# Optimization experiments

Measured on AMD Instinct MI355X. Metric: run time of the kernel, lower is better.

The kernel has to match this reference:

```python
import jax, jax.numpy as jnp
import numpy as np

B, S, D, H, M = 2, 2048, 1024, 16, 40
DH = D // H  # 64
L = S + M    # kv length after memory concat


def setup_inputs() -> dict:
    key = jax.random.key(0)
    ks = jax.random.split(key, 20)
    s = 1.0 / np.sqrt(D)
    inp = {
        'v': jax.random.normal(ks[0], (B, S, D), jnp.float32),
        'k': jax.random.normal(ks[1], (B, S, D), jnp.float32),
        'q': jax.random.normal(ks[2], (B, S, D), jnp.float32),
        # additive binary mask (1 = masked out), broadcast over heads
        'mask': jax.random.randint(ks[3], (B, 1, S, L), 0, 2).astype(jnp.float32),
        'Wq': jax.random.normal(ks[4], (D, D), jnp.float32) * s,
        'bq': jnp.zeros((D,), jnp.float32),
        'Wk': jax.random.normal(ks[5], (D, D), jnp.float32) * s,
        'bk': jnp.zeros((D,), jnp.float32),
        'Wv': jax.random.normal(ks[6], (D, D), jnp.float32) * s,
        'bv': jnp.zeros((D,), jnp.float32),
        'k_memory': jax.random.normal(ks[7], (1, M, D), jnp.float32) * (1.0 / np.sqrt(DH)),
        'v_memory': jax.random.normal(ks[8], (1, M, D), jnp.float32) * (1.0 / np.sqrt(M)),
        'Wkm': jax.random.normal(ks[9], (D, D), jnp.float32) * s,
        'bkm': jnp.zeros((D,), jnp.float32),
        'Wvm': jax.random.normal(ks[10], (D, D), jnp.float32) * s,
        'bvm': jnp.zeros((D,), jnp.float32),
        'Wo': jax.random.normal(ks[11], (D, D), jnp.float32) * s,
        'bo': jnp.zeros((D,), jnp.float32),
    }
    return inp


def _split_heads(x):
    # [B, T, D] -> [B, H, T, DH]
    b, t, _ = x.shape
    return x.reshape(b, t, H, DH).transpose(0, 2, 1, 3)


def reference(v, k, q, mask, Wq, bq, Wk, bk, Wv, bv, k_memory, v_memory,
              Wkm, bkm, Wvm, bvm, Wo, bo):
    qp = q @ Wq + bq
    kp = k @ Wk + bk
    vp = v @ Wv + bv
    km = (k_memory @ Wkm + bkm)  # [1, M, D]
    vm = (v_memory @ Wvm + bvm)  # [1, M, D]
    kc = jnp.concatenate([kp, jnp.broadcast_to(km, (kp.shape[0], M, D))], axis=1)
    vc = jnp.concatenate([vp, jnp.broadcast_to(vm, (vp.shape[0], M, D))], axis=1)
    qh, kh, vh = _split_heads(qp), _split_heads(kc), _split_heads(vc)
    # scores: [B, H, S, L]
    scores = jnp.einsum('bhqd,bhkd->bhqk', qh, kh) / np.sqrt(DH)
    scores = scores + mask * (-1e9)
    attn = jax.nn.softmax(scores, axis=-1)
    ctx = jnp.einsum('bhqk,bhkd->bhqd', attn, vh)  # [B, H, S, DH]
    ctx = ctx.transpose(0, 2, 1, 3).reshape(ctx.shape[0], S, D)
    out = ctx @ Wo + bo
    return (out, attn)
```

## Files before the change

### kernel.cpp

```cpp
#include <hip/hip_runtime.h>
#include <hip/hip_bf16.h>

typedef __attribute__((ext_vector_type(8))) short short8v;
typedef __attribute__((ext_vector_type(4))) short short4v;
typedef __attribute__((ext_vector_type(4))) float f32x4;

constexpr int B_ = 2, S_ = 2048, H_ = 16, MM_ = 40;
constexpr int L_ = S_ + MM_;
constexpr int LP_ = 2112;
constexpr int NT_ = 33;
constexpr float QSCALE = 0.18033688011112042f;

struct S2 { short hi, lo; };
__device__ __forceinline__ S2 split2(float f) {
    unsigned u = __builtin_bit_cast(unsigned, f);
    short hi = (short)(u >> 16);
    float fh = __builtin_bit_cast(float, u & 0xFFFF0000u);
    float fl = f - fh;
    short lo = (short)(__builtin_bit_cast(unsigned, fl) >> 16);
    return {hi, lo};
}
__device__ __forceinline__ short f2bh(float f) {
    unsigned u = __builtin_bit_cast(unsigned, f);
    u = (u + 0x7FFFu + ((u >> 16) & 1u)) >> 16;
    return (short)u;
}
__device__ __forceinline__ f32x4 mfma16(short8v a, short8v b, f32x4 c) {
    return __builtin_amdgcn_mfma_f32_16x16x32_bf16(a, b, c, 0, 0, 0);
}
__device__ __forceinline__ unsigned cvt_pk_bf16(float a, float b) {
    unsigned r;
    asm("v_cvt_pk_bf16_f32 %0, %1, %2" : "=v"(r) : "v"(a), "v"(b));
    return r;
}

__global__ __launch_bounds__(256) void wsplit6_kernel(
    const float* __restrict__ W0, const float* __restrict__ W1,
    const float* __restrict__ W2, const float* __restrict__ W3,
    const float* __restrict__ W4, const float* __restrict__ W5,
    short* __restrict__ WT)
{
    const float* Ws[6] = {W0, W1, W2, W3, W4, W5};
    const float* W = Ws[blockIdx.z];
    short* WTh = WT + (size_t)blockIdx.z * 2097152;
    short* WTl = WTh + 1048576;
    __shared__ float T[64][68];
    const int t = threadIdx.x;
    const int k0 = blockIdx.x * 64, n0 = blockIdx.y * 64;
    {
        int r = t >> 2, c = (t & 3) * 16;
        const float* src = W + (size_t)(k0 + r) * 1024 + n0 + c;
        *(float4*)&T[r][c + 0]  = *(const float4*)(src + 0);
        *(float4*)&T[r][c + 4]  = *(const float4*)(src + 4);
        *(float4*)&T[r][c + 8]  = *(const float4*)(src + 8);
        *(float4*)&T[r][c + 12] = *(const float4*)(src + 12);
    }
    __syncthreads();
    {
        int n = t >> 2, ks = (t & 3) * 16;
        short8v h0, h1, l0, l1;
#pragma unroll
        for (int j = 0; j < 8; ++j) {
            S2 a = split2(T[ks + j][n]);     h0[j] = a.hi; l0[j] = a.lo;
            S2 b = split2(T[ks + 8 + j][n]); h1[j] = b.hi; l1[j] = b.lo;
        }
        size_t dst = (size_t)(n0 + n) * 1024 + k0 + ks;
        *(short8v*)(WTh + dst) = h0;  *(short8v*)(WTh + dst + 8) = h1;
        *(short8v*)(WTl + dst) = l0;  *(short8v*)(WTl + dst + 8) = l1;
    }
}

template<int ASRC>
__device__ __forceinline__ void gemm_core(
    const float* __restrict__ Af, const short* __restrict__ Ahg,
    const short* __restrict__ Alg, const short* __restrict__ WTh,
    const short* __restrict__ WTl, const float* __restrict__ bias,
    float bscale, float scale,
    short* __restrict__ Oh, short* __restrict__ Ol, float* __restrict__ Of,
    int M, int RPB, int TD, int loff, int omode, int bx, int by,
    int kbeg, int kend)
{
    __shared__ short Ah[128][40];
    __shared__ short Al[128][40];
    __shared__ short Bh[128][40];
    __shared__ short Bl[128][40];
    const int tid = threadIdx.x;
    const int lane = tid & 63, wid = tid >> 6;
    const int wr = wid >> 1, wc = wid & 1;
    const int row0 = by * 128, col0 = bx * 128;
    const int sr = tid >> 1, sc = (tid & 1) << 4;

    f32x4 acc[4][4] = {};

    for (int k0 = kbeg; k0 < kend; k0 += 32) {
        if (ASRC == 0) {
            float f[16];
            int gr = row0 + sr;
            if (gr < M) {
                const float* ap = Af + (size_t)gr * 1024 + k0 + sc;
                float4 a0 = *(const float4*)(ap + 0);
                float4 a1 = *(const float4*)(ap + 4);
                float4 a2 = *(const float4*)(ap + 8);
                float4 a3 = *(const float4*)(ap + 12);
                f[0]=a0.x; f[1]=a0.y; f[2]=a0.z; f[3]=a0.w;
                f[4]=a1.x; f[5]=a1.y; f[6]=a1.z; f[7]=a1.w;
                f[8]=a2.x; f[9]=a2.y; f[10]=a2.z; f[11]=a2.w;
                f[12]=a3.x; f[13]=a3.y; f[14]=a3.z; f[15]=a3.w;
            } else {
#pragma unroll
                for (int j = 0; j < 16; ++j) f[j] = 0.f;
            }
            short8v h0, h1, l0, l1;
#pragma unroll
            for (int j = 0; j < 8; ++j) {
                S2 s = split2(f[j]); h0[j] = s.hi; l0[j] = s.lo;
            }
#pragma unroll
            for (int j = 0; j < 8; ++j) {
                S2 s = split2(f[8 + j]); h1[j] = s.hi; l1[j] = s.lo;
            }
            *(short8v*)&Ah[sr][sc] = h0; *(short8v*)&Ah[sr][sc + 8] = h1;
            *(short8v*)&Al[sr][sc] = l0; *(short8v*)&Al[sr][sc + 8] = l1;
        } else {
            const short* ah = Ahg + (size_t)(row0 + sr) * 1024 + k0 + sc;
            const short* al = Alg + (size_t)(row0 + sr) * 1024 + k0 + sc;
            *(short8v*)&Ah[sr][sc]     = *(const short8v*)ah;
            *(short8v*)&Ah[sr][sc + 8] = *(const short8v*)(ah + 8);
            *(short8v*)&Al[sr][sc]     = *(const short8v*)al;
            *(short8v*)&Al[sr][sc + 8] = *(const short8v*)(al + 8);
        }
        {
            const short* bh = WTh + (size_t)(col0 + sr) * 1024 + k0 + sc;
            const short* bl = WTl + (size_t)(col0 + sr) * 1024 + k0 + sc;
            *(short8v*)&Bh[sr][sc]     = *(const short8v*)bh;
            *(short8v*)&Bh[sr][sc + 8] = *(const short8v*)(bh + 8);
            *(short8v*)&Bl[sr][sc]     = *(const short8v*)bl;
            *(short8v*)&Bl[sr][sc + 8] = *(const short8v*)(bl + 8);
        }
        __syncthreads();
        const int kof = (lane >> 4) << 3;
        const int ar = lane & 15;
        short8v afh[4], afl[4], bfh[4], bfl[4];
#pragma unroll
        for (int i = 0; i < 4; ++i) {
            afh[i] = *(const short8v*)&Ah[wr * 64 + i * 16 + ar][kof];
            afl[i] = *(const short8v*)&Al[wr * 64 + i * 16 + ar][kof];
            bfh[i] = *(const short8v*)&Bh[wc * 64 + i * 16 + ar][kof];
            bfl[i] = *(const short8v*)&Bl[wc * 64 + i * 16 + ar][kof];
        }
#pragma unroll
        for (int i = 0; i < 4; ++i)
#pragma unroll
            for (int j = 0; j < 4; ++j) {
                acc[i][j] = mfma16(afh[i], bfh[j], acc[i][j]);
                acc[i][j] = mfma16(afh[i], bfl[j], acc[i][j]);
                acc[i][j] = mfma16(afl[i], bfh[j], acc[i][j]);
            }
        __syncthreads();
    }

#pragma unroll
    for (int i = 0; i < 4; ++i) {
#pragma unroll
        for (int j = 0; j < 4; ++j) {
            int colb = col0 + wc * 64 + j * 16 + (lane & 15);
            float bv = bias[colb] * bscale;
            int rowb = row0 + wr * 64 + i * 16 + ((lane >> 4) << 2);
            if (omode == 2) {
                if (rowb < M) {
                    int bb = rowb / RPB, tt = rowb % RPB;
                    int hh = colb >> 6, dh = colb & 63;
                    short4v hs;
#pragma unroll
                    for (int r = 0; r < 4; ++r)
                        hs[r] = f2bh((acc[i][j][r] + bv) * scale);
                    size_t dst = ((size_t)(bb * H_ + hh) * 64 + dh) * LP_ + loff + tt;
                    *(short4v*)(Oh + dst) = hs;
                }
            } else {
#pragma unroll
                for (int r = 0; r < 4; ++r) {
                    int row = rowb + r;
                    if (row < M) {
                        float o = (acc[i][j][r] + bv) * scale;
                        int bb = row / RPB, tt = row % RPB;
                        if (omode == 0) {
                            Of[((size_t)bb * TD + loff + tt) * 1024 + colb] = o;
                        } else {
                            int hh = colb >> 6, dh = colb & 63;
                            size_t dst = ((size_t)(bb * H_ + hh) * TD + loff + tt) * 64 + dh;
                            S2 s = split2(o);
                            Oh[dst] = s.hi; Ol[dst] = s.lo;
                        }
                    }
                }
            }
        }
    }
}

__global__ __launch_bounds__(256) void qkv_gemm(
    const float* __restrict__ q_in, const float* __restrict__ k_in,
    const float* __restrict__ v_in, const float* __restrict__ kmem,
    const float* __restrict__ vmem, const short* __restrict__ WT,
    const float* __restrict__ bq, const float* __restrict__ bk,
    const float* __restrict__ bv, const float* __restrict__ bkm,
    const float* __restrict__ bvm,
    short* __restrict__ Qh, short* __restrict__ Ql,
    short* __restrict__ Kh, short* __restrict__ Kl, short* __restrict__ Vh,
    const float* __restrict__ mask, unsigned* __restrict__ mp)
{
    const int z = blockIdx.z;
    if (z == 0) {
        const int blk = blockIdx.y * 8 + blockIdx.x;
        for (int rr = 0; rr < 16; ++rr) {
            const int row = blk * 16 + rr;
            const float* mr = mask + (size_t)row * L_;
            unsigned* orow = mp + (size_t)row * 68;
            for (int wd = threadIdx.x; wd < 66; wd += 256) {
                int l0 = wd * 32;
                unsigned bits = 0u;
                int lim = (wd < 65) ? 32 : 8;
                for (int j = 0; j < lim; j += 4) {
                    float4 m4 = *(const float4*)(mr + l0 + j);
                    bits |= ((unsigned)(m4.x != 0.f)) << (j + 0);
                    bits |= ((unsigned)(m4.y != 0.f)) << (j + 1);
                    bits |= ((unsigned)(m4.z != 0.f)) << (j + 2);
                    bits |= ((unsigned)(m4.w != 0.f)) << (j + 3);
                }
                if (wd == 65) bits |= 0xFFFFFF00u;
                orow[wd] = bits;
            }
        }
        for (int k = threadIdx.x; k < 192; k += 256) {
            int g = blk * 192 + k;
            int rd = g / 24, l = L_ + g % 24;
            Vh[(size_t)rd * LP_ + l] = 0;
        }
        return;
    }
    if (z >= 4) {
        if (blockIdx.y != 0) return;
        const int which = (z - 4) >> 1, b = (z - 4) & 1;
        const float* A = which ? vmem : kmem;
        const short* WTh = WT + (size_t)(3 + which) * 2097152;
        const short* WTl = WTh + 1048576;
        const float* bias = which ? bvm : bkm;
        short* Oh = which ? (Vh + (size_t)b * H_ * 64 * LP_)
                          : (Kh + (size_t)b * H_ * LP_ * 64);
        short* Ol = which ? nullptr : (Kl + (size_t)b * H_ * LP_ * 64);
        gemm_core<0>(A, nullptr, nullptr, WTh, WTl, bias, 1.0f, 1.0f,
                     Oh, Ol, nullptr, 40, 40, LP_, S_, which ? 2 : 1,
                     blockIdx.x, 0, 0, 1024);
        return;
    }
    const int g = z - 1;
    const float* A = (g == 0) ? q_in : (g == 1) ? k_in : v_in;
    const short* WTh = WT + (size_t)g * 2097152;
    const short* WTl = WTh + 1048576;
    const float* bias = (g == 0) ? bq : (g == 1) ? bk : bv;
    float scale = (g == 0) ? QSCALE : 1.0f;
    short* Oh = (g == 0) ? Qh : (g == 1) ? Kh : Vh;
    short* Ol = (g == 0) ? Ql : Kl;
    int omode = (g == 2) ? 2 : 1;
    int TD = (g == 0) ? S_ : LP_;
    gemm_core<0>(A, nullptr, nullptr, WTh, WTl, bias, 1.0f, scale,
                 Oh, Ol, nullptr, 4096, 2048, TD, 0, omode,
                 blockIdx.x, blockIdx.y, 0, 1024);
}

__global__ __launch_bounds__(256) void out_gemm(
    const short* __restrict__ Ch, const short* __restrict__ Cl,
    const short* __restrict__ WT, const float* __restrict__ bo,
    float* __restrict__ Po0, float* __restrict__ Po1)
{
    const int z = blockIdx.z;
    const short* WTh = WT + (size_t)5 * 2097152;
    gemm_core<1>(nullptr, Ch, Cl, WTh, WTh + 1048576, bo,
                 z == 0 ? 1.0f : 0.0f, 1.0f,
                 nullptr, nullptr, z == 0 ? Po0 : Po1, 4096, 2048, S_, 0, 0,
                 blockIdx.x, blockIdx.y, z * 512, z * 512 + 512);
}

__global__ __launch_bounds__(256) void add_out(
    const float* __restrict__ Po0, const float* __restrict__ Po1,
    float* __restrict__ outp)
{
    int i = (blockIdx.x * 256 + threadIdx.x) * 4;
    float4 a = *(const float4*)(Po0 + i);
    float4 b = *(const float4*)(Po1 + i);
    a.x += b.x; a.y += b.y; a.z += b.z; a.w += b.w;
    *(float4*)(outp + i) = a;
}

__global__ __launch_bounds__(256) void attn4_kernel(
    const short* __restrict__ Qh, const short* __restrict__ Ql,
    const short* __restrict__ Kh, const short* __restrict__ Kl,
    const short* __restrict__ Vh, const unsigned* __restrict__ mp,
    float* __restrict__ attn,
    short* __restrict__ Ch, short* __restrict__ Cl)
{
    __shared__ short KhB[2][64][64];
    __shared__ short KlB[2][64][64];
    __shared__ short VB[64][64];
    __shared__ short Ph[4][16][68];

    const int id = blockIdx.x;
    const int wg = (id & 7) * 64 + (id >> 3);
    const int bh = wg >> 4, qb2 = wg & 15;
    const int b = bh >> 4, h = bh & 15;
    const int lane = threadIdx.x & 63, w = threadIdx.x >> 6;
    const int lq = lane & 15, hi = lane >> 4;
    const int sw = lq & 7;
    const int q0A = qb2 * 128 + w * 16;
    const int q0B = q0A + 64;

    const char* kh_g = (const char*)(Kh + (size_t)bh * LP_ * 64);
    const char* kl_g = (const char*)(Kl + (size_t)bh * LP_ * 64);
    const char* v_g  = (const char*)(Vh + (size_t)bh * 64 * LP_);

    auto stage_k = [&](int buf, int tt) {
#pragma unroll
        for (int i = 0; i < 2; ++i) {
            int o = w * 2048 + i * 1024 + lane * 16;
            int r = o >> 7, c = (o >> 4) & 7;
            int cs = c ^ (r & 7);
            const char* sh = kh_g + (size_t)tt * 8192 + r * 128 + cs * 16;
            const char* sl = kl_g + (size_t)tt * 8192 + r * 128 + cs * 16;
            __builtin_amdgcn_global_load_lds((const void*)sh,
                (void*)((char*)&KhB[buf][0][0] + w * 2048 + i * 1024), 16, 0, 0);
            __builtin_amdgcn_global_load_lds((const void*)sl,
                (void*)((char*)&KlB[buf][0][0] + w * 2048 + i * 1024), 16, 0, 0);
        }
    };
    auto stage_v = [&](int tt) {
#pragma unroll
        for (int i = 0; i < 2; ++i) {
            int o = w * 2048 + i * 1024 + lane * 16;
            int dh = o >> 7, c = (o >> 4) & 7;
            int cs = c ^ (dh & 7);
            const char* src = v_g + (size_t)dh * (LP_ * 2) + (size_t)tt * 128 + cs * 16;
            __builtin_amdgcn_global_load_lds((const void*)src,
                (void*)((char*)&VB[0][0] + w * 2048 + i * 1024), 16, 0, 0);
        }
    };

    const size_t qbA = ((size_t)bh * S_ + q0A + lq) * 64 + hi * 8;
    const size_t qbB = ((size_t)bh * S_ + q0B + lq) * 64 + hi * 8;
    const short8v qh0A = *(const short8v*)(Qh + qbA);
    const short8v qh1A = *(const short8v*)(Qh + qbA + 32);
    const short8v ql0A = *(const short8v*)(Ql + qbA);
    const short8v ql1A = *(const short8v*)(Ql + qbA + 32);
    const short8v qh0B = *(const short8v*)(Qh + qbB);
    const short8v qh1B = *(const short8v*)(Qh + qbB + 32);
    const short8v ql0B = *(const short8v*)(Ql + qbB);
    const short8v ql1B = *(const short8v*)(Ql + qbB + 32);
    const unsigned* mrowA = mp + ((size_t)b * S_ + q0A + lq) * 68;
    const unsigned* mrowB = mp + ((size_t)b * S_ + q0B + lq) * 68;

    const int dr = lane >> 2, dc = lane & 3;
    short* dbaseA = (short*)(attn + ((size_t)bh * S_ + q0A + dr) * L_);
    short* dbaseB = (short*)(attn + ((size_t)bh * S_ + q0B + dr) * L_);

    float smA = 0.f, smB = 0.f;
    f32x4 pvA[4] = {};
    f32x4 pvB[4] = {};

    stage_k(0, 0);
    stage_v(0);
    __syncthreads();

    int cur = 0;
    for (int t = 0; t < NT_; ++t) {
        if (t < NT_ - 1) stage_k(cur ^ 1, t + 1);

        const short8v* kp = (const short8v*)&KhB[cur][0][0];
        const short8v* lp = (const short8v*)&KlB[cur][0][0];
        short8v kh0s[4], kh1s[4], kl0s[4], kl1s[4];
#pragma unroll
        for (int ls = 0; ls < 4; ++ls) {
            const int r = ls * 16 + lq;
            kh0s[ls] = kp[r * 8 + (hi ^ sw)];
            kh1s[ls] = kp[r * 8 + ((hi + 4) ^ sw)];
            kl0s[ls] = lp[r * 8 + (hi ^ sw)];
            kl1s[ls] = lp[r * 8 + ((hi + 4) ^ sw)];
        }
        const unsigned w0A = mrowA[2 * t], w1A = mrowA[2 * t + 1];
#pragma unroll
        for (int ls = 0; ls < 4; ++ls) {
            __builtin_amdgcn_s_setprio(1);
            f32x4 acc = {0.f, 0.f, 0.f, 0.f};
            acc = mfma16(kh0s[ls], qh0A, acc); acc = mfma16(kh1s[ls], qh1A, acc);
            acc = mfma16(kh0s[ls], ql0A, acc); acc = mfma16(kh1s[ls], ql1A, acc);
            acc = mfma16(kl0s[ls], qh0A, acc); acc = mfma16(kl1s[ls], qh1A, acc);
            __builtin_amdgcn_s_setprio(0);
            const unsigned wb = (ls & 2) ? w1A : w0A;
            const int sh = (ls & 1) * 16 + hi * 4;
            float pr[4];
#pragma unroll
            for (int r2 = 0; r2 < 4; ++r2) {
                float e = __builtin_exp2f(acc[r2]);
                pr[r2] = ((wb >> (sh + r2)) & 1u) ? 0.f : e;
            }
            smA += (pr[0] + pr[1]) + (pr[2] + pr[3]);
            *(uint2*)&Ph[w][lq][ls * 16 + hi * 4] =
                uint2{cvt_pk_bf16(pr[0], pr[1]), cvt_pk_bf16(pr[2], pr[3])};
        }
        {
            short8v v0 = *(const short8v*)&Ph[w][dr][dc * 8];
            short8v v1 = *(const short8v*)&Ph[w][dr][32 + dc * 8];
            short* dst = dbaseA + t * 64 + dc * 8;
            if (t < NT_ - 1) { *(short8v*)dst = v0; *(short8v*)(dst + 32) = v1; }
            else { *(short8v*)dst = v0; if (dc == 0) *(short8v*)(dst + 32) = v1; }
        }
        __syncthreads();
        {
            const short8v pa0 = *(const short8v*)&Ph[w][lq][hi * 8];
            const short8v pa1 = *(const short8v*)&Ph[w][lq][32 + hi * 8];
            const short8v* vp = (const short8v*)&VB[0][0];
            __builtin_amdgcn_s_setprio(1);
#pragma unroll
            for (int j = 0; j < 4; ++j)
                pvA[j] = mfma16(pa0, vp[(j * 16 + lq) * 8 + (hi ^ sw)], pvA[j]);
#pragma unroll
            for (int j = 0; j < 4; ++j)
                pvA[j] = mfma16(pa1, vp[(j * 16 + lq) * 8 + ((hi + 4) ^ sw)], pvA[j]);
            __builtin_amdgcn_s_setprio(0);
        }
        const unsigned w0B = mrowB[2 * t], w1B = mrowB[2 * t + 1];
#pragma unroll
        for (int ls = 0; ls < 4; ++ls) {
            __builtin_amdgcn_s_setprio(1);
            f32x4 acc = {0.f, 0.f, 0.f, 0.f};
            acc = mfma16(kh0s[ls], qh0B, acc); acc = mfma16(kh1s[ls], qh1B, acc);
            acc = mfma16(kh0s[ls], ql0B, acc); acc = mfma16(kh1s[ls], ql1B, acc);
            acc = mfma16(kl0s[ls], qh0B, acc); acc = mfma16(kl1s[ls], qh1B, acc);
            __builtin_amdgcn_s_setprio(0);
            const unsigned wb = (ls & 2) ? w1B : w0B;
            const int sh = (ls & 1) * 16 + hi * 4;
            float pr[4];
#pragma unroll
            for (int r2 = 0; r2 < 4; ++r2) {
                float e = __builtin_exp2f(acc[r2]);
                pr[r2] = ((wb >> (sh + r2)) & 1u) ? 0.f : e;
            }
            smB += (pr[0] + pr[1]) + (pr[2] + pr[3]);
            *(uint2*)&Ph[w][lq][ls * 16 + hi * 4] =
                uint2{cvt_pk_bf16(pr[0], pr[1]), cvt_pk_bf16(pr[2], pr[3])};
        }
        {
            short8v v0 = *(const short8v*)&Ph[w][dr][dc * 8];
            short8v v1 = *(const short8v*)&Ph[w][dr][32 + dc * 8];
            short* dst = dbaseB + t * 64 + dc * 8;
            if (t < NT_ - 1) { *(short8v*)dst = v0; *(short8v*)(dst + 32) = v1; }
            else { *(short8v*)dst = v0; if (dc == 0) *(short8v*)(dst + 32) = v1; }
        }
        {
            const short8v pa0 = *(const short8v*)&Ph[w][lq][hi * 8];
            const short8v pa1 = *(const short8v*)&Ph[w][lq][32 + hi * 8];
            const short8v* vp = (const short8v*)&VB[0][0];
            __builtin_amdgcn_s_setprio(1);
#pragma unroll
            for (int j = 0; j < 4; ++j)
                pvB[j] = mfma16(pa0, vp[(j * 16 + lq) * 8 + (hi ^ sw)], pvB[j]);
#pragma unroll
            for (int j = 0; j < 4; ++j)
                pvB[j] = mfma16(pa1, vp[(j * 16 + lq) * 8 + ((hi + 4) ^ sw)], pvB[j]);
            __builtin_amdgcn_s_setprio(0);
        }
        __syncthreads();
        if (t < NT_ - 1) stage_v(t + 1);
        cur ^= 1;
    }

    smA += __shfl_xor(smA, 16); smA += __shfl_xor(smA, 32);
    smB += __shfl_xor(smB, 16); smB += __shfl_xor(smB, 32);

#pragma unroll
    for (int r = 0; r < 4; ++r) {
        float svA = __shfl(smA, hi * 4 + r);
        float svB = __shfl(smB, hi * 4 + r);
        float ivA = svA > 0.f ? 1.0f / svA : 0.f;
        float ivB = svB > 0.f ? 1.0f / svB : 0.f;
#pragma unroll
        for (int j = 0; j < 4; ++j) {
            size_t dA = ((size_t)b * S_ + q0A + hi * 4 + r) * 1024 + h * 64 + j * 16 + lq;
            S2 sA = split2(pvA[j][r] * ivA);
            Ch[dA] = sA.hi; Cl[dA] = sA.lo;
            size_t dB = ((size_t)b * S_ + q0B + hi * 4 + r) * 1024 + h * 64 + j * 16 + lq;
            S2 sB = split2(pvB[j][r] * ivB);
            Ch[dB] = sB.hi; Cl[dB] = sB.lo;
        }
    }

    asm volatile("s_waitcnt vmcnt(0)");
#pragma unroll 1
    for (int s = 0; s < 2; ++s) {
        const int q0 = s ? q0B : q0A;
        const float smv = s ? smB : smA;
#pragma unroll 1
        for (int i = 0; i < 16; ++i) {
            float sv = __shfl(smv, i);
            float iv = sv > 0.f ? 1.0f / sv : 0.f;
            float* rowf = attn + ((size_t)bh * S_ + q0 + i) * L_;
            unsigned* rw = (unsigned*)rowf;
            unsigned u[17];
#pragma unroll
            for (int it = 0; it < 16; ++it) u[it] = rw[lane + it * 64];
            if (lane < 20) u[16] = rw[lane + 1024];
#pragma unroll
            for (int it = 0; it < 16; ++it) {
                unsigned uu = u[it];
                float2 v;
                v.x = __builtin_bit_cast(float, uu << 16) * iv;
                v.y = __builtin_bit_cast(float, uu & 0xFFFF0000u) * iv;
                *(float2*)(rowf + 2 * (lane + it * 64)) = v;
            }
            if (lane < 20) {
                unsigned uu = u[16];
                float2 v;
                v.x = __builtin_bit_cast(float, uu << 16) * iv;
                v.y = __builtin_bit_cast(float, uu & 0xFFFF0000u) * iv;
                *(float2*)(rowf + 2 * (lane + 1024)) = v;
            }
        }
    }
}

extern "C" void kernel_launch(void* const* d_in, const int* in_sizes, int n_in,
                              void* d_out, int out_size, void* d_ws, size_t ws_size,
                              hipStream_t stream)
{
    const float* v_in = (const float*)d_in[0];
    const float* k_in = (const float*)d_in[1];
    const float* q_in = (const float*)d_in[2];
    const float* mask = (const float*)d_in[3];
    const float* Wq = (const float*)d_in[4];  const float* bq = (const float*)d_in[5];
    const float* Wk = (const float*)d_in[6];  const float* bk = (const float*)d_in[7];
    const float* Wv = (const float*)d_in[8];  const float* bv = (const float*)d_in[9];
    const float* kmem = (const float*)d_in[10];
    const float* vmem = (const float*)d_in[11];
    const float* Wkm = (const float*)d_in[12]; const float* bkm = (const float*)d_in[13];
    const float* Wvm = (const float*)d_in[14]; const float* bvm = (const float*)d_in[15];
    const float* Wo = (const float*)d_in[16];  const float* bo = (const float*)d_in[17];

    char* wsb = (char*)d_ws;
    short* WT  = (short*)(wsb);
    short* Qhb = (short*)(wsb + 25165824);
    short* Qlb = (short*)(wsb + 33554432);
    short* Khb = (short*)(wsb + 41943040);
    short* Klb = (short*)(wsb + 50593792);
    short* Vhb = (short*)(wsb + 59244544);
    short* Chb = (short*)(wsb + 67895296);
    short* Clb = (short*)(wsb + 76283904);
    unsigned* mp = (unsigned*)(wsb + 84934656);
    if (ws_size < 86048768) return;
    float* Po0 = (float*)(wsb + 25165824);
    float* Po1 = (float*)(wsb + 41943040);

    float* outp = (float*)d_out;
    float* attnp = outp + (size_t)B_ * S_ * 1024;

    dim3 blk(256);

    wsplit6_kernel<<<dim3(16, 16, 6), blk, 0, stream>>>(Wq, Wk, Wv, Wkm, Wvm, Wo, WT);

    qkv_gemm<<<dim3(8, 32, 8), blk, 0, stream>>>(
        q_in, k_in, v_in, kmem, vmem, WT, bq, bk, bv, bkm, bvm,
        Qhb, Qlb, Khb, Klb, Vhb, mask, mp);

    attn4_kernel<<<dim3(512), blk, 0, stream>>>(
        Qhb, Qlb, Khb, Klb, Vhb, mp, attnp, Chb, Clb);

    out_gemm<<<dim3(8, 32, 2), blk, 0, stream>>>(Chb, Clb, WT, bo, Po0, Po1);
    add_out<<<dim3(4096), blk, 0, stream>>>(Po0, Po1, outp);
}
```

Before: 571.6 us.

## Move attn renormalization into a tail kernel co-scheduled with the output GEMM

The attention kernel no longer rescales its bf16 probability rows into fp32 at the end. It writes the per-row inverse sums to a workspace buffer instead. A new tail kernel merges the output-projection GEMM blocks with blocks that read the bf16 rows and write the normalized fp32 attention, so that memory-bound pass can overlap with GEMM compute and the attention kernel's tail shortens. V fragments are also loaded from LDS once per tile and reused for both query halves, which raises register pressure.

```diff
diff --git a/kernel.cpp b/kernel.cpp
--- a/kernel.cpp
+++ b/kernel.cpp
@@ -269,35 +269,11 @@
                  blockIdx.x, blockIdx.y, 0, 1024);
 }
 
-__global__ __launch_bounds__(256) void out_gemm(
-    const short* __restrict__ Ch, const short* __restrict__ Cl,
-    const short* __restrict__ WT, const float* __restrict__ bo,
-    float* __restrict__ Po0, float* __restrict__ Po1)
-{
-    const int z = blockIdx.z;
-    const short* WTh = WT + (size_t)5 * 2097152;
-    gemm_core<1>(nullptr, Ch, Cl, WTh, WTh + 1048576, bo,
-                 z == 0 ? 1.0f : 0.0f, 1.0f,
-                 nullptr, nullptr, z == 0 ? Po0 : Po1, 4096, 2048, S_, 0, 0,
-                 blockIdx.x, blockIdx.y, z * 512, z * 512 + 512);
-}
-
-__global__ __launch_bounds__(256) void add_out(
-    const float* __restrict__ Po0, const float* __restrict__ Po1,
-    float* __restrict__ outp)
-{
-    int i = (blockIdx.x * 256 + threadIdx.x) * 4;
-    float4 a = *(const float4*)(Po0 + i);
-    float4 b = *(const float4*)(Po1 + i);
-    a.x += b.x; a.y += b.y; a.z += b.z; a.w += b.w;
-    *(float4*)(outp + i) = a;
-}
-
 __global__ __launch_bounds__(256) void attn4_kernel(
     const short* __restrict__ Qh, const short* __restrict__ Ql,
     const short* __restrict__ Kh, const short* __restrict__ Kl,
     const short* __restrict__ Vh, const unsigned* __restrict__ mp,
-    float* __restrict__ attn,
+    float* __restrict__ attn, float* __restrict__ invg,
     short* __restrict__ Ch, short* __restrict__ Cl)
 {
     __shared__ short KhB[2][64][64];
@@ -414,17 +390,23 @@
             else { *(short8v*)dst = v0; if (dc == 0) *(short8v*)(dst + 32) = v1; }
         }
         __syncthreads();
+        short8v vf0[4], vf1[4];
+        {
+            const short8v* vp = (const short8v*)&VB[0][0];
+#pragma unroll
+            for (int j = 0; j < 4; ++j) {
+                vf0[j] = vp[(j * 16 + lq) * 8 + (hi ^ sw)];
+                vf1[j] = vp[(j * 16 + lq) * 8 + ((hi + 4) ^ sw)];
+            }
+        }
         {
             const short8v pa0 = *(const short8v*)&Ph[w][lq][hi * 8];
             const short8v pa1 = *(const short8v*)&Ph[w][lq][32 + hi * 8];
-            const short8v* vp = (const short8v*)&VB[0][0];
             __builtin_amdgcn_s_setprio(1);
 #pragma unroll
-            for (int j = 0; j < 4; ++j)
-                pvA[j] = mfma16(pa0, vp[(j * 16 + lq) * 8 + (hi ^ sw)], pvA[j]);
-#pragma unroll
-            for (int j = 0; j < 4; ++j)
-                pvA[j] = mfma16(pa1, vp[(j * 16 + lq) * 8 + ((hi + 4) ^ sw)], pvA[j]);
+            for (int j = 0; j < 4; ++j) pvA[j] = mfma16(pa0, vf0[j], pvA[j]);
+#pragma unroll
+            for (int j = 0; j < 4; ++j) pvA[j] = mfma16(pa1, vf1[j], pvA[j]);
             __builtin_amdgcn_s_setprio(0);
         }
         const unsigned w0B = mrowB[2 * t], w1B = mrowB[2 * t + 1];
@@ -458,14 +440,11 @@
         {
             const short8v pa0 = *(const short8v*)&Ph[w][lq][hi * 8];
             const short8v pa1 = *(const short8v*)&Ph[w][lq][32 + hi * 8];
-            const short8v* vp = (const short8v*)&VB[0][0];
             __builtin_amdgcn_s_setprio(1);
 #pragma unroll
-            for (int j = 0; j < 4; ++j)
-                pvB[j] = mfma16(pa0, vp[(j * 16 + lq) * 8 + (hi ^ sw)], pvB[j]);
-#pragma unroll
-            for (int j = 0; j < 4; ++j)
-                pvB[j] = mfma16(pa1, vp[(j * 16 + lq) * 8 + ((hi + 4) ^ sw)], pvB[j]);
+            for (int j = 0; j < 4; ++j) pvB[j] = mfma16(pa0, vf0[j], pvB[j]);
+#pragma unroll
+            for (int j = 0; j < 4; ++j) pvB[j] = mfma16(pa1, vf1[j], pvB[j]);
             __builtin_amdgcn_s_setprio(0);
         }
         __syncthreads();
@@ -475,6 +454,10 @@
 
     smA += __shfl_xor(smA, 16); smA += __shfl_xor(smA, 32);
     smB += __shfl_xor(smB, 16); smB += __shfl_xor(smB, 32);
+    if (lane < 16) {
+        invg[(size_t)bh * S_ + q0A + lane] = smA > 0.f ? 1.0f / smA : 0.f;
+        invg[(size_t)bh * S_ + q0B + lane] = smB > 0.f ? 1.0f / smB : 0.f;
+    }
 
 #pragma unroll
     for (int r = 0; r < 4; ++r) {
@@ -492,39 +475,64 @@
             Ch[dB] = sB.hi; Cl[dB] = sB.lo;
         }
     }
-
-    asm volatile("s_waitcnt vmcnt(0)");
+}
+
+__global__ __launch_bounds__(256) void tail_kernel(
+    const short* __restrict__ Ch, const short* __restrict__ Cl,
+    const short* __restrict__ WT, const float* __restrict__ bo,
+    float* __restrict__ Po0, float* __restrict__ Po1,
+    float* __restrict__ attn, const float* __restrict__ invg)
+{
+    const int blk = blockIdx.x;
+    if (blk < 512) {
+        const int z = blk >> 8, r = blk & 255;
+        const short* WTh = WT + (size_t)5 * 2097152;
+        gemm_core<1>(nullptr, Ch, Cl, WTh, WTh + 1048576, bo,
+                     z == 0 ? 1.0f : 0.0f, 1.0f,
+                     nullptr, nullptr, z == 0 ? Po0 : Po1, 4096, 2048, S_, 0, 0,
+                     r & 7, r >> 3, z * 512, z * 512 + 512);
+        return;
+    }
+    const int nb = blk - 512;
+    const int lane = threadIdx.x & 63, w = threadIdx.x >> 6;
 #pragma unroll 1
-    for (int s = 0; s < 2; ++s) {
-        const int q0 = s ? q0B : q0A;
-        const float smv = s ? smB : smA;
-#pragma unroll 1
-        for (int i = 0; i < 16; ++i) {
-            float sv = __shfl(smv, i);
-            float iv = sv > 0.f ? 1.0f / sv : 0.f;
-            float* rowf = attn + ((size_t)bh * S_ + q0 + i) * L_;
-            unsigned* rw = (unsigned*)rowf;
-            unsigned u[17];
-#pragma unroll
-            for (int it = 0; it < 16; ++it) u[it] = rw[lane + it * 64];
-            if (lane < 20) u[16] = rw[lane + 1024];
-#pragma unroll
-            for (int it = 0; it < 16; ++it) {
-                unsigned uu = u[it];
-                float2 v;
-                v.x = __builtin_bit_cast(float, uu << 16) * iv;
-                v.y = __builtin_bit_cast(float, uu & 0xFFFF0000u) * iv;
-                *(float2*)(rowf + 2 * (lane + it * 64)) = v;
-            }
-            if (lane < 20) {
-                unsigned uu = u[16];
-                float2 v;
-                v.x = __builtin_bit_cast(float, uu << 16) * iv;
-                v.y = __builtin_bit_cast(float, uu & 0xFFFF0000u) * iv;
-                *(float2*)(rowf + 2 * (lane + 1024)) = v;
-            }
-        }
-    }
+    for (int i = 0; i < 8; ++i) {
+        const int row = nb * 32 + w * 8 + i;
+        const float iv = invg[row];
+        float* rowf = attn + (size_t)row * L_;
+        unsigned* rw = (unsigned*)rowf;
+        unsigned u[17];
+#pragma unroll
+        for (int it = 0; it < 16; ++it) u[it] = rw[lane + it * 64];
+        if (lane < 20) u[16] = rw[lane + 1024];
+        asm volatile("s_waitcnt vmcnt(0)" ::: "memory");
+#pragma unroll
+        for (int it = 0; it < 16; ++it) {
+            unsigned uu = u[it];
+            float2 v;
+            v.x = __builtin_bit_cast(float, uu << 16) * iv;
+            v.y = __builtin_bit_cast(float, uu & 0xFFFF0000u) * iv;
+            *(float2*)(rowf + 2 * (lane + it * 64)) = v;
+        }
+        if (lane < 20) {
+            unsigned uu = u[16];
+            float2 v;
+            v.x = __builtin_bit_cast(float, uu << 16) * iv;
+            v.y = __builtin_bit_cast(float, uu & 0xFFFF0000u) * iv;
+            *(float2*)(rowf + 2 * (lane + 1024)) = v;
+        }
+    }
+}
+
+__global__ __launch_bounds__(256) void add_out(
+    const float* __restrict__ Po0, const float* __restrict__ Po1,
+    float* __restrict__ outp)
+{
+    int i = (blockIdx.x * 256 + threadIdx.x) * 4;
+    float4 a = *(const float4*)(Po0 + i);
+    float4 b = *(const float4*)(Po1 + i);
+    a.x += b.x; a.y += b.y; a.z += b.z; a.w += b.w;
+    *(float4*)(outp + i) = a;
 }
 
 extern "C" void kernel_launch(void* const* d_in, const int* in_sizes, int n_in,
@@ -553,6 +561,7 @@
     short* Vhb = (short*)(wsb + 59244544);
     short* Chb = (short*)(wsb + 67895296);
     short* Clb = (short*)(wsb + 76283904);
+    float* invb = (float*)(wsb + 84672512);
     unsigned* mp = (unsigned*)(wsb + 84934656);
     if (ws_size < 86048768) return;
     float* Po0 = (float*)(wsb + 25165824);
@@ -570,8 +579,10 @@
         Qhb, Qlb, Khb, Klb, Vhb, mask, mp);
 
     attn4_kernel<<<dim3(512), blk, 0, stream>>>(
-        Qhb, Qlb, Khb, Klb, Vhb, mp, attnp, Chb, Clb);
-
-    out_gemm<<<dim3(8, 32, 2), blk, 0, stream>>>(Chb, Clb, WT, bo, Po0, Po1);
+        Qhb, Qlb, Khb, Klb, Vhb, mp, attnp, invb, Chb, Clb);
+
+    tail_kernel<<<dim3(2560), blk, 0, stream>>>(
+        Chb, Clb, WT, bo, Po0, Po1, attnp, invb);
+
     add_out<<<dim3(4096), blk, 0, stream>>>(Po0, Po1, outp);
 }
```

Measured after the change: 575.3 us. No clear change (+0.6%).
